# Optimization experiments

Hardware: AMD Instinct MI355X
Metric: run time of the kernel (lower is better)

Reference implementation:

```python
import jax, jax.numpy as jnp
import numpy as np
from jax import lax

INPUT, HIDDEN, LAYERS = 256, 512, 3
SEQ, BATCH = 1024, 32
STDV = 1.0 / float(np.sqrt(HIDDEN))


def _uniform(key, shape):
    return jax.random.uniform(key, shape, jnp.float32, -STDV, STDV)


def setup_inputs() -> dict:
    key = jax.random.key(0)
    ks = iter(jax.random.split(key, 64))
    x = jax.random.normal(next(ks), (SEQ, BATCH, INPUT), jnp.float32)
    H3 = 3 * HIDDEN
    # layer 0: input dim = INPUT; layers 1..2: input dim = 2*HIDDEN
    w_ih_l0 = _uniform(next(ks), (2, H3, INPUT))          # (dir, 3H, in)
    w_hh_l0 = _uniform(next(ks), (2, H3, HIDDEN))
    b_ih_l0 = _uniform(next(ks), (2, H3))
    b_hh_l0 = _uniform(next(ks), (2, H3))
    w_ih_lr = _uniform(next(ks), (LAYERS - 1, 2, H3, 2 * HIDDEN))
    w_hh_lr = _uniform(next(ks), (LAYERS - 1, 2, H3, HIDDEN))
    b_ih_lr = _uniform(next(ks), (LAYERS - 1, 2, H3))
    b_hh_lr = _uniform(next(ks), (LAYERS - 1, 2, H3))
    return dict(x=x, w_ih_l0=w_ih_l0, w_hh_l0=w_hh_l0, b_ih_l0=b_ih_l0,
                b_hh_l0=b_hh_l0, w_ih_lr=w_ih_lr, w_hh_lr=w_hh_lr,
                b_ih_lr=b_ih_lr, b_hh_lr=b_hh_lr)


def _gru_dir(xs, w_ih, w_hh, b_ih, b_hh, reverse):
    # xs: (T, B, in); precompute input projection for the whole sequence
    Xi = jnp.einsum('tbi,gi->tbg', xs, w_ih) + b_ih  # (T, B, 3H)
    h0 = jnp.zeros((xs.shape[1], HIDDEN), xs.dtype)

    def step(h, xi):
        hp = h @ w_hh.T + b_hh                       # (B, 3H)
        ir, iz, inn = jnp.split(xi, 3, axis=-1)
        hr, hz, hn = jnp.split(hp, 3, axis=-1)
        r = jax.nn.sigmoid(ir + hr)
        z = jax.nn.sigmoid(iz + hz)
        n = jnp.tanh(inn + r * hn)
        h_new = (1.0 - z) * n + z * h
        return h_new, h_new

    h_last, ys = lax.scan(step, h0, Xi, reverse=reverse)
    return h_last, ys  # ys in original time order even when reverse=True


def reference(x, w_ih_l0, w_hh_l0, b_ih_l0, b_hh_l0,
              w_ih_lr, w_hh_lr, b_ih_lr, b_hh_lr):
    layer_input = x
    h_n = []
    for layer in range(LAYERS):
        if layer == 0:
            wi, wh, bi, bh = w_ih_l0, w_hh_l0, b_ih_l0, b_hh_l0
        else:
            wi, wh = w_ih_lr[layer - 1], w_hh_lr[layer - 1]
            bi, bh = b_ih_lr[layer - 1], b_hh_lr[layer - 1]
        hf, yf = _gru_dir(layer_input, wi[0], wh[0], bi[0], bh[0], reverse=False)
        hb, yb = _gru_dir(layer_input, wi[1], wh[1], bi[1], bh[1], reverse=True)
        h_n.append(hf)
        h_n.append(hb)
        layer_input = jnp.concatenate([yf, yb], axis=-1)  # (T, B, 2H)
    return jnp.stack(h_n, axis=0)  # (LAYERS*2, B, H)
```

## Files before the change

kernel.cpp:

```cpp
#include <hip/hip_runtime.h>
#include <stdint.h>

#define SEQ   1024
#define BATCH 32
#define HID   512
#define G3    1536
#define NW    32
#define JPW   16
#define THREADS 256
#define FSTR  256
#define CSTR  64
#define CH    16
#define NCH   64
#define NG    192
#define NPROD 192
#define SPIN_MAX 65536

typedef __attribute__((ext_vector_type(8))) short  short8;
typedef __attribute__((ext_vector_type(4))) float  f32x4;
typedef __attribute__((ext_vector_type(4))) unsigned short us4;
typedef unsigned long long ull;

__device__ __forceinline__ unsigned short f2bf(float f) {
  union { float f; unsigned int u; } v; v.f = f;
  unsigned int u = v.u;
  return (unsigned short)((u + 0x7FFFu + ((u >> 16) & 1u)) >> 16);
}
__device__ __forceinline__ float bf2f(unsigned short u) {
  union { unsigned int i; float f; } v; v.i = ((unsigned int)u) << 16; return v.f;
}
__device__ __forceinline__ short8 pack8(const float* __restrict__ p) {
  short8 o;
#pragma unroll
  for (int i = 0; i < 8; i++) o[i] = (short)f2bf(p[i]);
  return o;
}
__device__ __forceinline__ f32x4 mfma16(short8 a, short8 b, f32x4 c) {
  return __builtin_amdgcn_mfma_f32_16x16x32_bf16(a, b, c, 0, 0, 0);
}

__global__ void cvt_wb(const float* __restrict__ w, short8* __restrict__ out, int kcx, int nc) {
  int c = blockIdx.x * blockDim.x + threadIdx.x;
  if (c >= nc) return;
  int lane = c & 63, r = c >> 6;
  int kc = r % kcx, ng = r / kcx;
  int n   = ng * 16 + (lane & 15);
  int col = kc * 32 + (lane >> 4) * 8;
  int K = kcx * 32;
  out[c] = pack8(w + (size_t)n * K + col);
}

template<int KCX, bool WRITE_Y>
__global__ __launch_bounds__(THREADS, 1) void gru_mega(
    const void* __restrict__ Ain,
    short8* __restrict__ yout,
    const short8* __restrict__ wb,
    const float* __restrict__ whh,
    const float* __restrict__ bih,
    const float* __restrict__ bhh,
    us4* __restrict__ Xic,
    short8* __restrict__ hbuf,
    int* __restrict__ pflags,
    int* __restrict__ cflags,
    int* __restrict__ prodcnt,
    float* __restrict__ hout)
{
  __shared__ f32x4 pbuf[768];
  __shared__ ull   xbuf3[384];

  const int tid  = threadIdx.x;
  const int lane = tid & 63;
  const int wave = tid >> 6;
  const int quad = lane >> 4;
  const int l15  = lane & 15;
  const int bx   = blockIdx.x;
  const int sub  = bx & 7;

  if (sub >= 2) {
    const int p    = (bx >> 3) * 6 + (sub - 2);
    const int tg   = p & 15;
    const int ngg  = p >> 4;
    const int dirp = (ngg >= 6) ? 1 : 0;
    int* fl = cflags + dirp * NW * FSTR;

    for (int c = 0; c < NCH; c++) {
      const int tgt = (c >= 2) ? CH * (c - 1) : 0;
      if (wave == 0) {
        int it = 0;
        while (true) {
          int v = (lane < NW)
                    ? __hip_atomic_load(&fl[lane * FSTR], __ATOMIC_RELAXED, __HIP_MEMORY_SCOPE_AGENT)
                    : tgt;
          if (__all(v >= tgt)) break;
          if (++it > SPIN_MAX) break;
          __builtin_amdgcn_s_sleep(16);
        }
      }
      __syncthreads();
      const int sl = tg;
      const int s  = c * CH + sl;
      const int t  = dirp ? (SEQ - 1 - s) : s;
      for (int mi2 = 0; mi2 < 2; mi2++) {
        short8 a[KCX];
        if constexpr (KCX == 8) {
          const float* xr = (const float*)Ain + ((size_t)t * 32 + mi2 * 16 + l15) * 256 + quad * 8;
#pragma unroll
          for (int kc = 0; kc < KCX; kc++) a[kc] = pack8(xr + kc * 32);
        } else {
          const short8* ap = (const short8*)Ain + ((size_t)(t * 2 + mi2) * KCX) * 64 + lane;
#pragma unroll
          for (int kc = 0; kc < KCX; kc++) a[kc] = ap[kc * 64];
        }
        for (int ng = ngg * 16 + wave; ng < ngg * 16 + 16; ng += 4) {
          const short8* bp = wb + (size_t)ng * KCX * 64 + lane;
          f32x4 ac0 = (f32x4){0.f, 0.f, 0.f, 0.f};
          f32x4 ac1 = (f32x4){0.f, 0.f, 0.f, 0.f};
#pragma unroll
          for (int kc = 0; kc < KCX; kc += 2) {
            ac0 = mfma16(a[kc],     bp[kc * 64],       ac0);
            ac1 = mfma16(a[kc + 1], bp[(kc + 1) * 64], ac1);
          }
          const int n  = ng * 16 + l15;
          const int gg = (ng % 96) >> 5;
          const float bias = bih[n] + (gg < 2 ? bhh[n] : 0.f);
          us4 o;
#pragma unroll
          for (int r = 0; r < 4; r++) o[r] = f2bf(ac0[r] + ac1[r] + bias);
          us4* dst = Xic + ((((size_t)(c & 1)) * CH + sl) * NG + ng) * 128 + mi2 * 64 + lane;
          asm volatile("global_store_dwordx2 %0, %1, off sc0 sc1" :: "v"(dst), "v"(o) : "memory");
        }
      }
      asm volatile("s_waitcnt vmcnt(0)" ::: "memory");
      __syncthreads();
      if (tid == 0)
        __hip_atomic_fetch_add(&prodcnt[c * CSTR], 1, __ATOMIC_RELAXED, __HIP_MEMORY_SCOPE_AGENT);
    }
    return;
  }

  const int mi  = wave & 1;
  const int kh  = wave >> 1;
  const int dir = sub;
  const int wg  = bx >> 3;
  const int j0  = wg * JPW;
  const bool rev = (dir == 1);

  short8 wh[3][8];
  {
    const float* pwd = whh + (size_t)dir * G3 * HID;
#pragma unroll
    for (int g = 0; g < 3; g++) {
      const float* pw = pwd + (size_t)(g * HID + j0 + l15) * HID + quad * 8;
#pragma unroll
      for (int c = 0; c < 8; c++) wh[g][c] = pack8(pw + (kh * 8 + c) * 32);
    }
  }
  const float bhn = bhh[dir * G3 + 2 * HID + j0 + (tid & 15)];
  f32x4 hreg = (f32x4){0.f, 0.f, 0.f, 0.f};

  int* pfl = pflags + dir * 32;
  int* cfl = cflags + dir * NW * FSTR;
  char* hb = (char*)(hbuf + (size_t)dir * 2 * 2048);

  for (int s = 0; s < SEQ; s++) {
    const int t  = rev ? (SEQ - 1 - s) : s;
    const int c  = s >> 4;
    const int sl = s & 15;

    const int xig = (wave >= 1) ? (wave - 1) : 0;
    const char* xp = (const char*)Xic
        + (((((size_t)(c & 1)) * CH + sl) * NG + (dir * 96 + xig * 32 + wg)) * 128 + lane) * 8;
    ull xi0 = 0, xi1 = 0;
    if (wave >= 1 && sl != 0)
      asm volatile(
          "global_load_dwordx2 %0, %2, off sc0 sc1\n\t"
          "global_load_dwordx2 %1, %2, off offset:512 sc0 sc1\n\t"
          "s_waitcnt vmcnt(0)"
          : "=&v"(xi0), "=&v"(xi1) : "v"(xp) : "memory");

    if (wave == 0) {
      int* fp = pfl + (lane & 31);
      int it = 0;
      while (true) {
        int v = s;
        if (s > 0)
          asm volatile("global_load_dword %0, %1, off sc0 sc1\n\ts_waitcnt vmcnt(0)"
                       : "=v"(v) : "v"(fp) : "memory");
        bool ok = __all(v >= s);
        if (ok && sl == 0) {
          int cnt = __hip_atomic_load(&prodcnt[c * CSTR], __ATOMIC_RELAXED, __HIP_MEMORY_SCOPE_AGENT);
          ok = (cnt >= NPROD);
        }
        if (ok) break;
        if (++it > SPIN_MAX) break;
        __builtin_amdgcn_s_sleep(1);
      }
    }
    __syncthreads();
    if (wave >= 1 && sl == 0)
      asm volatile(
          "global_load_dwordx2 %0, %2, off sc0 sc1\n\t"
          "global_load_dwordx2 %1, %2, off offset:512 sc0 sc1\n\t"
          "s_waitcnt vmcnt(0)"
          : "=&v"(xi0), "=&v"(xi1) : "v"(xp) : "memory");

    f32x4 p0 = (f32x4){0.f, 0.f, 0.f, 0.f};
    f32x4 p1 = (f32x4){0.f, 0.f, 0.f, 0.f};
    f32x4 p2 = (f32x4){0.f, 0.f, 0.f, 0.f};
    if (s > 0) {
      const char* hp = hb + (size_t)((s - 1) & 1) * 32768 + (size_t)mi * 16384
                     + (size_t)kh * 8192 + (size_t)lane * 16;
      short8 a0, a1, a2, a3, a4, a5, a6, a7;
      asm volatile(
          "global_load_dwordx4 %0, %8, off sc0 sc1\n\t"
          "global_load_dwordx4 %1, %8, off offset:1024 sc0 sc1\n\t"
          "global_load_dwordx4 %2, %8, off offset:2048 sc0 sc1\n\t"
          "global_load_dwordx4 %3, %8, off offset:3072 sc0 sc1\n\t"
          "global_load_dwordx4 %4, %9, off sc0 sc1\n\t"
          "global_load_dwordx4 %5, %9, off offset:1024 sc0 sc1\n\t"
          "global_load_dwordx4 %6, %9, off offset:2048 sc0 sc1\n\t"
          "global_load_dwordx4 %7, %9, off offset:3072 sc0 sc1\n\t"
          "s_waitcnt vmcnt(0)"
          : "=&v"(a0), "=&v"(a1), "=&v"(a2), "=&v"(a3),
            "=&v"(a4), "=&v"(a5), "=&v"(a6), "=&v"(a7)
          : "v"(hp), "v"(hp + 4096) : "memory");
      p0 = mfma16(a0, wh[0][0], p0); p1 = mfma16(a0, wh[1][0], p1); p2 = mfma16(a0, wh[2][0], p2);
      p0 = mfma16(a1, wh[0][1], p0); p1 = mfma16(a1, wh[1][1], p1); p2 = mfma16(a1, wh[2][1], p2);
      p0 = mfma16(a2, wh[0][2], p0); p1 = mfma16(a2, wh[1][2], p1); p2 = mfma16(a2, wh[2][2], p2);
      p0 = mfma16(a3, wh[0][3], p0); p1 = mfma16(a3, wh[1][3], p1); p2 = mfma16(a3, wh[2][3], p2);
      p0 = mfma16(a4, wh[0][4], p0); p1 = mfma16(a4, wh[1][4], p1); p2 = mfma16(a4, wh[2][4], p2);
      p0 = mfma16(a5, wh[0][5], p0); p1 = mfma16(a5, wh[1][5], p1); p2 = mfma16(a5, wh[2][5], p2);
      p0 = mfma16(a6, wh[0][6], p0); p1 = mfma16(a6, wh[1][6], p1); p2 = mfma16(a6, wh[2][6], p2);
      p0 = mfma16(a7, wh[0][7], p0); p1 = mfma16(a7, wh[1][7], p1); p2 = mfma16(a7, wh[2][7], p2);
    }

    {
      const int idx0 = mi * 64 + quad * 16 + l15;
      pbuf[kh * 384 + idx0]       = p0;
      pbuf[kh * 384 + 128 + idx0] = p1;
      pbuf[kh * 384 + 256 + idx0] = p2;
      if (wave >= 1) {
        xbuf3[xig * 128 + lane]      = xi0;
        xbuf3[xig * 128 + 64 + lane] = xi1;
      }
    }
    __syncthreads();

    if (tid < 128) {
      const int gmi = tid >> 6, gq = (tid >> 4) & 3, gj = tid & 15;
      const int kg  = j0 + gj;
      const int rb  = gmi * 64 + gq * 16 + gj;
      f32x4 s0 = pbuf[rb]       + pbuf[384 + rb];
      f32x4 s1 = pbuf[128 + rb] + pbuf[512 + rb];
      f32x4 s2 = pbuf[256 + rb] + pbuf[640 + rb];
      const ull xr_ = xbuf3[rb];
      const ull xz_ = xbuf3[128 + rb];
      const ull xn_ = xbuf3[256 + rb];
      f32x4 hnew;
#pragma unroll
      for (int r = 0; r < 4; r++) {
        float rr  = 1.f / (1.f + __expf(-(s0[r] + bf2f((unsigned short)(xr_ >> (16 * r))))));
        float zz  = 1.f / (1.f + __expf(-(s1[r] + bf2f((unsigned short)(xz_ >> (16 * r))))));
        float px  = bf2f((unsigned short)(xn_ >> (16 * r)));
        float a2v = px + rr * (s2[r] + bhn);
        float ex  = __expf(2.f * a2v);
        float nn  = 1.f - 2.f / (ex + 1.f);
        hnew[r] = (1.f - zz) * nn + zz * hreg[r];
      }
      hreg = hnew;
      const int kc = kg >> 5;
      const int qq = (kg >> 3) & 3;
      char* pdst = hb + (size_t)(s & 1) * 32768 + (size_t)gmi * 16384
                 + (size_t)kc * 1024 + (size_t)(qq * 16 + gq * 4) * 16 + (size_t)(kg & 7) * 2;
#pragma unroll
      for (int r = 0; r < 4; r++) {
        unsigned int uv = (unsigned int)f2bf(hnew[r]);
        asm volatile("global_store_short %0, %1, off sc0 sc1" :: "v"(pdst + r * 16), "v"(uv) : "memory");
      }
      if (WRITE_Y) {
        char* yb = (char*)yout
            + ((((size_t)(t * 2 + gmi)) * 32 + (dir << 4) + kc) * 64 + qq * 16 + gq * 4) * 16
            + (size_t)(kg & 7) * 2;
#pragma unroll
        for (int r = 0; r < 4; r++)
          *(unsigned short*)(yb + r * 16) = f2bf(hnew[r]);
      }
      if (s == SEQ - 1) {
#pragma unroll
        for (int r = 0; r < 4; r++)
          hout[((size_t)dir * 32 + gmi * 16 + gq * 4 + r) * HID + kg] = hnew[r];
      }
    }
    asm volatile("s_waitcnt vmcnt(0)" ::: "memory");
    __syncthreads();
    if (tid == 0) {
      const int fv = s + 1;
      int* fpd = pfl + wg;
      asm volatile("global_store_dword %0, %1, off sc0 sc1" :: "v"(fpd), "v"(fv) : "memory");
      if (sl == 15)
        __hip_atomic_store(&cfl[wg * FSTR], fv, __ATOMIC_RELAXED, __HIP_MEMORY_SCOPE_AGENT);
    }
  }
}

extern "C" void kernel_launch(void* const* d_in, const int* in_sizes, int n_in,
                              void* d_out, int out_size, void* d_ws, size_t ws_size,
                              hipStream_t stream)
{
  const float* x       = (const float*)d_in[0];
  const float* w_ih_l0 = (const float*)d_in[1];
  const float* w_hh_l0 = (const float*)d_in[2];
  const float* b_ih_l0 = (const float*)d_in[3];
  const float* b_hh_l0 = (const float*)d_in[4];
  const float* w_ih_lr = (const float*)d_in[5];
  const float* w_hh_lr = (const float*)d_in[6];
  const float* b_ih_lr = (const float*)d_in[7];
  const float* b_hh_lr = (const float*)d_in[8];
  float* out = (float*)d_out;

  char* ws = (char*)d_ws;
  size_t off = 0;
  auto alloc = [&](size_t bytes) {
    char* p = ws + off;
    off += (bytes + 255) & ~(size_t)255;
    return p;
  };
  short8* y0   = (short8*)alloc((size_t)SEQ * 2 * 32 * 64 * 16);
  short8* y1   = (short8*)alloc((size_t)SEQ * 2 * 32 * 64 * 16);
  short8* wb   = (short8*)alloc((size_t)NG * 32 * 64 * 16);
  short8* hbuf = (short8*)alloc((size_t)2 * 2 * 2048 * 16);
  int*    pflags  = (int*)alloc((size_t)3 * 64 * 4);
  int*    cflags  = (int*)alloc((size_t)3 * 2 * NW * FSTR * 4);
  int*    prodcnt = (int*)alloc((size_t)3 * NCH * CSTR * 4);
  us4*    Xic  = (us4*)alloc((size_t)2 * CH * NG * 2 * 64 * 8);

  hipMemsetAsync(pflags,  0, (size_t)3 * 64 * 4, stream);
  hipMemsetAsync(cflags,  0, (size_t)3 * 2 * NW * FSTR * 4, stream);
  hipMemsetAsync(prodcnt, 0, (size_t)3 * NCH * CSTR * 4, stream);

  {
    int nc = NG * 8 * 64;
    cvt_wb<<<(nc + 255) / 256, 256, 0, stream>>>(w_ih_l0, wb, 8, nc);
    gru_mega<8, true><<<256, THREADS, 0, stream>>>(
        x, y0, wb, w_hh_l0, b_ih_l0, b_hh_l0, Xic, hbuf,
        pflags, cflags, prodcnt, out);
  }
  {
    int nc = NG * 32 * 64;
    cvt_wb<<<(nc + 255) / 256, 256, 0, stream>>>(w_ih_lr, wb, 32, nc);
    gru_mega<32, true><<<256, THREADS, 0, stream>>>(
        y0, y1, wb, w_hh_lr, b_ih_lr, b_hh_lr, Xic, hbuf,
        pflags + 64, cflags + 2 * NW * FSTR,
        prodcnt + NCH * CSTR, out + 2 * BATCH * HID);
  }
  {
    int nc = NG * 32 * 64;
    cvt_wb<<<(nc + 255) / 256, 256, 0, stream>>>(w_ih_lr + (size_t)2 * G3 * 1024, wb, 32, nc);
    gru_mega<32, false><<<256, THREADS, 0, stream>>>(
        y1, nullptr, wb, w_hh_lr + (size_t)2 * G3 * HID,
        b_ih_lr + 2 * G3, b_hh_lr + 2 * G3, Xic, hbuf,
        pflags + 128, cflags + 4 * NW * FSTR,
        prodcnt + 2 * NCH * CSTR, out + 4 * BATCH * HID);
  }
}
```

Before: 11.80 ms.

## Spread gate math over all threads and pad per-step flags to separate lines

The per-step flags move from a packed 32-int array to one flag per workgroup padded by FSTR, and are read and written with agent-scope atomics. The aim is to keep producers writing separate cache lines and avoid false sharing while other workgroups poll. The gate nonlinearity is now spread over all 256 threads, each handling two hidden units for one batch row, instead of 128 threads handling four rows each. This shortens the serial per-step epilogue, and h and y are written as packed 32-bit stores rather than 16-bit shorts, at the cost of more scalar LDS reads.

```diff
diff --git a/kernel.cpp b/kernel.cpp
--- a/kernel.cpp
+++ b/kernel.cpp
@@ -60,7 +60,7 @@
     const float* __restrict__ bhh,
     us4* __restrict__ Xic,
     short8* __restrict__ hbuf,
-    int* __restrict__ pflags,
+    int* __restrict__ flags,
     int* __restrict__ cflags,
     int* __restrict__ prodcnt,
     float* __restrict__ hout)
@@ -155,10 +155,11 @@
       for (int c = 0; c < 8; c++) wh[g][c] = pack8(pw + (kh * 8 + c) * 32);
     }
   }
-  const float bhn = bhh[dir * G3 + 2 * HID + j0 + (tid & 15)];
-  f32x4 hreg = (f32x4){0.f, 0.f, 0.f, 0.f};
-
-  int* pfl = pflags + dir * 32;
+  const float bhn0 = bhh[dir * G3 + 2 * HID + j0 + 2 * (tid & 7)];
+  const float bhn1 = bhh[dir * G3 + 2 * HID + j0 + 2 * (tid & 7) + 1];
+  float hr0 = 0.f, hr1 = 0.f;
+
+  int* fl  = flags  + dir * NW * FSTR;
   int* cfl = cflags + dir * NW * FSTR;
   char* hb = (char*)(hbuf + (size_t)dir * 2 * 2048);
 
@@ -179,13 +180,11 @@
           : "=&v"(xi0), "=&v"(xi1) : "v"(xp) : "memory");
 
     if (wave == 0) {
-      int* fp = pfl + (lane & 31);
       int it = 0;
       while (true) {
-        int v = s;
-        if (s > 0)
-          asm volatile("global_load_dword %0, %1, off sc0 sc1\n\ts_waitcnt vmcnt(0)"
-                       : "=v"(v) : "v"(fp) : "memory");
+        int v = (s > 0 && lane < NW)
+                  ? __hip_atomic_load(&fl[lane * FSTR], __ATOMIC_RELAXED, __HIP_MEMORY_SCOPE_AGENT)
+                  : s;
         bool ok = __all(v >= s);
         if (ok && sl == 0) {
           int cnt = __hip_atomic_load(&prodcnt[c * CSTR], __ATOMIC_RELAXED, __HIP_MEMORY_SCOPE_AGENT);
@@ -246,57 +245,54 @@
     }
     __syncthreads();
 
-    if (tid < 128) {
-      const int gmi = tid >> 6, gq = (tid >> 4) & 3, gj = tid & 15;
-      const int kg  = j0 + gj;
-      const int rb  = gmi * 64 + gq * 16 + gj;
-      f32x4 s0 = pbuf[rb]       + pbuf[384 + rb];
-      f32x4 s1 = pbuf[128 + rb] + pbuf[512 + rb];
-      f32x4 s2 = pbuf[256 + rb] + pbuf[640 + rb];
-      const ull xr_ = xbuf3[rb];
-      const ull xz_ = xbuf3[128 + rb];
-      const ull xn_ = xbuf3[256 + rb];
-      f32x4 hnew;
-#pragma unroll
-      for (int r = 0; r < 4; r++) {
-        float rr  = 1.f / (1.f + __expf(-(s0[r] + bf2f((unsigned short)(xr_ >> (16 * r))))));
-        float zz  = 1.f / (1.f + __expf(-(s1[r] + bf2f((unsigned short)(xz_ >> (16 * r))))));
-        float px  = bf2f((unsigned short)(xn_ >> (16 * r)));
-        float a2v = px + rr * (s2[r] + bhn);
+    {
+      const int b  = tid >> 3;
+      const int jj = tid & 7;
+      const int gmi = b >> 4, gq = (b >> 2) & 3, r = b & 3;
+      float h2[2];
+      float hprev[2] = {hr0, hr1};
+      float bhn2[2]  = {bhn0, bhn1};
+#pragma unroll
+      for (int e = 0; e < 2; e++) {
+        const int j  = 2 * jj + e;
+        const int rb = gmi * 64 + gq * 16 + j;
+        float s0 = pbuf[rb][r]       + pbuf[384 + rb][r];
+        float s1 = pbuf[128 + rb][r] + pbuf[512 + rb][r];
+        float s2 = pbuf[256 + rb][r] + pbuf[640 + rb][r];
+        float xr_ = bf2f((unsigned short)(xbuf3[rb]       >> (16 * r)));
+        float xz_ = bf2f((unsigned short)(xbuf3[128 + rb] >> (16 * r)));
+        float xn_ = bf2f((unsigned short)(xbuf3[256 + rb] >> (16 * r)));
+        float rr  = 1.f / (1.f + __expf(-(s0 + xr_)));
+        float zz  = 1.f / (1.f + __expf(-(s1 + xz_)));
+        float a2v = xn_ + rr * (s2 + bhn2[e]);
         float ex  = __expf(2.f * a2v);
         float nn  = 1.f - 2.f / (ex + 1.f);
-        hnew[r] = (1.f - zz) * nn + zz * hreg[r];
-      }
-      hreg = hnew;
-      const int kc = kg >> 5;
-      const int qq = (kg >> 3) & 3;
-      char* pdst = hb + (size_t)(s & 1) * 32768 + (size_t)gmi * 16384
-                 + (size_t)kc * 1024 + (size_t)(qq * 16 + gq * 4) * 16 + (size_t)(kg & 7) * 2;
-#pragma unroll
-      for (int r = 0; r < 4; r++) {
-        unsigned int uv = (unsigned int)f2bf(hnew[r]);
-        asm volatile("global_store_short %0, %1, off sc0 sc1" :: "v"(pdst + r * 16), "v"(uv) : "memory");
-      }
+        h2[e] = (1.f - zz) * nn + zz * hprev[e];
+      }
+      hr0 = h2[0]; hr1 = h2[1];
+      unsigned int val = (unsigned int)f2bf(h2[0]) | ((unsigned int)f2bf(h2[1]) << 16);
+      const int k   = j0 + 2 * jj;
+      const int kc  = k >> 5;
+      const int q   = (k >> 3) & 3;
+      const int l16 = (b & 15) + (q << 4);
+      const int mib = b >> 4;
+      char* pdst = hb + (size_t)(s & 1) * 32768 + (size_t)mib * 16384
+                 + (size_t)kc * 1024 + (size_t)l16 * 16 + (size_t)(k & 7) * 2;
+      asm volatile("global_store_dword %0, %1, off sc0 sc1" :: "v"(pdst), "v"(val) : "memory");
       if (WRITE_Y) {
-        char* yb = (char*)yout
-            + ((((size_t)(t * 2 + gmi)) * 32 + (dir << 4) + kc) * 64 + qq * 16 + gq * 4) * 16
-            + (size_t)(kg & 7) * 2;
-#pragma unroll
-        for (int r = 0; r < 4; r++)
-          *(unsigned short*)(yb + r * 16) = f2bf(hnew[r]);
+        size_t yb = (((size_t)(t * 2 + mib) * 32 + (dir << 4) + kc) * 64 + l16) * 16 + (size_t)(k & 7) * 2;
+        *(unsigned int*)((char*)yout + yb) = val;
       }
       if (s == SEQ - 1) {
-#pragma unroll
-        for (int r = 0; r < 4; r++)
-          hout[((size_t)dir * 32 + gmi * 16 + gq * 4 + r) * HID + kg] = hnew[r];
+        hout[((size_t)dir * 32 + b) * HID + k]     = h2[0];
+        hout[((size_t)dir * 32 + b) * HID + k + 1] = h2[1];
       }
     }
     asm volatile("s_waitcnt vmcnt(0)" ::: "memory");
     __syncthreads();
     if (tid == 0) {
       const int fv = s + 1;
-      int* fpd = pfl + wg;
-      asm volatile("global_store_dword %0, %1, off sc0 sc1" :: "v"(fpd), "v"(fv) : "memory");
+      __hip_atomic_store(&fl[wg * FSTR], fv, __ATOMIC_RELAXED, __HIP_MEMORY_SCOPE_AGENT);
       if (sl == 15)
         __hip_atomic_store(&cfl[wg * FSTR], fv, __ATOMIC_RELAXED, __HIP_MEMORY_SCOPE_AGENT);
     }
@@ -329,12 +325,12 @@
   short8* y1   = (short8*)alloc((size_t)SEQ * 2 * 32 * 64 * 16);
   short8* wb   = (short8*)alloc((size_t)NG * 32 * 64 * 16);
   short8* hbuf = (short8*)alloc((size_t)2 * 2 * 2048 * 16);
-  int*    pflags  = (int*)alloc((size_t)3 * 64 * 4);
+  int*    flags   = (int*)alloc((size_t)3 * 2 * NW * FSTR * 4);
   int*    cflags  = (int*)alloc((size_t)3 * 2 * NW * FSTR * 4);
   int*    prodcnt = (int*)alloc((size_t)3 * NCH * CSTR * 4);
   us4*    Xic  = (us4*)alloc((size_t)2 * CH * NG * 2 * 64 * 8);
 
-  hipMemsetAsync(pflags,  0, (size_t)3 * 64 * 4, stream);
+  hipMemsetAsync(flags,   0, (size_t)3 * 2 * NW * FSTR * 4, stream);
   hipMemsetAsync(cflags,  0, (size_t)3 * 2 * NW * FSTR * 4, stream);
   hipMemsetAsync(prodcnt, 0, (size_t)3 * NCH * CSTR * 4, stream);
 
@@ -343,14 +339,14 @@
     cvt_wb<<<(nc + 255) / 256, 256, 0, stream>>>(w_ih_l0, wb, 8, nc);
     gru_mega<8, true><<<256, THREADS, 0, stream>>>(
         x, y0, wb, w_hh_l0, b_ih_l0, b_hh_l0, Xic, hbuf,
-        pflags, cflags, prodcnt, out);
+        flags, cflags, prodcnt, out);
   }
   {
     int nc = NG * 32 * 64;
     cvt_wb<<<(nc + 255) / 256, 256, 0, stream>>>(w_ih_lr, wb, 32, nc);
     gru_mega<32, true><<<256, THREADS, 0, stream>>>(
         y0, y1, wb, w_hh_lr, b_ih_lr, b_hh_lr, Xic, hbuf,
-        pflags + 64, cflags + 2 * NW * FSTR,
+        flags + 2 * NW * FSTR, cflags + 2 * NW * FSTR,
         prodcnt + NCH * CSTR, out + 2 * BATCH * HID);
   }
   {
@@ -359,7 +355,7 @@
     gru_mega<32, false><<<256, THREADS, 0, stream>>>(
         y1, nullptr, wb, w_hh_lr + (size_t)2 * G3 * HID,
         b_ih_lr + 2 * G3, b_hh_lr + 2 * G3, Xic, hbuf,
-        pflags + 128, cflags + 4 * NW * FSTR,
+        flags + 4 * NW * FSTR, cflags + 4 * NW * FSTR,
         prodcnt + 2 * NCH * CSTR, out + 4 * BATCH * HID);
   }
 }
```

Result: faster. 11.01 ms (-6.7%).
